# Kernel optimization log

Hardware: AMD Instinct MI355X
Metric: run time of the kernel (lower is better)

## Reference

```python
import jax, jax.numpy as jnp
import numpy as np

N = 1_000_000
HID = 128

def setup_inputs() -> dict:
    key = jax.random.key(0)
    ks = jax.random.split(key, 4)
    F = jnp.eye(2, dtype=jnp.float32)[None] + 0.1 * jax.random.normal(ks[0], (N, 2, 2), dtype=jnp.float32)
    W1 = jax.random.normal(ks[1], (7, HID), dtype=jnp.float32) * (1.0 / np.sqrt(7))
    b1 = jnp.zeros((HID,), dtype=jnp.float32)
    W2 = jax.random.normal(ks[2], (HID, HID), dtype=jnp.float32) * (1.0 / np.sqrt(HID))
    b2 = jnp.zeros((HID,), dtype=jnp.float32)
    W3 = jax.random.normal(ks[3], (HID, 4), dtype=jnp.float32) * (1.0 / np.sqrt(HID))
    b3 = jnp.zeros((4,), dtype=jnp.float32)
    return {"F": F, "W1": W1, "b1": b1, "W2": W2, "b2": b2, "W3": W3, "b3": b3}

def reference(F, W1, b1, W2, b2, W3, b3):
    F = F.reshape(-1, 2, 2)                      # [N,2,2]
    U, sigma, Vh = jnp.linalg.svd(F)             # batched 2x2 SVD
    R = jnp.matmul(U, Vh)                        # rotation part, [N,2,2]
    FtF = jnp.einsum('nij,nik->njk', F, F)       # F^T F, [N,2,2]
    I = jnp.eye(2, dtype=F.dtype)
    I1 = sigma - 1.0                             # [N,2]
    I2 = (FtF - I).reshape(-1, 4)                # [N,4]
    det = F[:, 0, 0] * F[:, 1, 1] - F[:, 0, 1] * F[:, 1, 0]
    I3 = det[:, None] - 1.0                      # [N,1]
    inv = jnp.concatenate([I1, I2, I3], axis=1)  # [N,7]
    h = jax.nn.relu(inv @ W1 + b1)
    h = jax.nn.relu(h @ W2 + b2)
    x = (h @ W3 + b3).reshape(-1, 2, 2)
    x = (x + jnp.swapaxes(x, 1, 2)) * 0.5        # symmetrize
    delta_Fp = jnp.matmul(R, x)
    return delta_Fp + F
```

## Files before the change

### kernel.cpp

```cpp
#include <hip/hip_runtime.h>

typedef _Float16 f16x8 __attribute__((ext_vector_type(8)));
typedef _Float16 f16x2 __attribute__((ext_vector_type(2)));
typedef __fp16   fp16x2r __attribute__((ext_vector_type(2)));
typedef float    f32x4 __attribute__((ext_vector_type(4)));

#define MFMA(a, b, c) __builtin_amdgcn_mfma_f32_16x16x32_f16((a), (b), (c), 0, 0, 0)

__device__ inline f16x8 zero8() {
    f16x8 z;
#pragma unroll
    for (int i = 0; i < 8; ++i) z[i] = (_Float16)0.0f;
    return z;
}

__global__ __launch_bounds__(256, 1)
void DeformationCorrector_78967268704761_kernel(
        const float* __restrict__ F,
        const float* __restrict__ W1, const float* __restrict__ b1,
        const float* __restrict__ W2, const float* __restrict__ b2,
        const float* __restrict__ W3, const float* __restrict__ b3,
        float* __restrict__ out, int N)
{
    __shared__ __align__(16) _Float16 W2f[8][4][64][8];
    __shared__ __align__(16) _Float16 W1f[8][16][8];
    __shared__ __align__(16) _Float16 W3c[4][16][8];
    __shared__ __align__(16) _Float16 invL[256][8];
    __shared__ __align__(16) _Float16 scratch[4][64][40];

    const int tid  = threadIdx.x;
    const int lane = tid & 63;
    const int w    = tid >> 6;
    const int l15  = tid & 15;
    const int quad = (tid >> 4) & 3;

    for (int m = tid; m < 128 * 128; m += 256) {
        int k = m >> 7, n = m & 127;
        W2f[n >> 4][k >> 5][((k >> 3) & 3) * 16 + (n & 15)][k & 7] = (_Float16)W2[m];
    }
    for (int f = tid; f < 1024; f += 256) {
        int nt = f >> 7, n15 = (f >> 3) & 15, j = f & 7;
        W1f[nt][n15][j] = (_Float16)((j < 7) ? W1[j * 128 + nt * 16 + n15]
                                             : b1[nt * 16 + n15]);
    }
    for (int f = tid; f < 512; f += 256) {
        int s = f >> 7, idx = (f >> 3) & 15, j = f & 7;
        int q = idx >> 2, n3 = idx & 3;
        int ch = s * 32 + (j & 1) * 16 + q * 4 + (j >> 1);
        W3c[s][idx][j] = (_Float16)W3[ch * 4 + n3];
    }
    float b2r[8];
#pragma unroll
    for (int nt = 0; nt < 8; ++nt) b2r[nt] = b2[nt * 16 + l15];
    const float b3v = (l15 < 4) ? b3[l15] : 0.f;
    __syncthreads();

    const int ntiles = (N + 255) >> 8;
    const int stride = (int)gridDim.x;

    float a, b, c, d;
    {
        const int p0 = blockIdx.x * 256 + tid;
        if (blockIdx.x < ntiles && p0 < N) {
            const float4 f4 = *(const float4*)(F + 4ll * p0);
            a = f4.x; b = f4.y; c = f4.z; d = f4.w;
        } else { a = 1.f; b = 0.f; c = 0.f; d = 1.f; }
    }

    for (int tile = blockIdx.x; tile < ntiles; tile += stride) {
        float na = 1.f, nb = 0.f, nc = 0.f, nd = 1.f;
        {
            const int pn = (tile + stride) * 256 + tid;
            if (tile + stride < ntiles && pn < N) {
                const float4 f4 = *(const float4*)(F + 4ll * pn);
                na = f4.x; nb = f4.y; nc = f4.z; nd = f4.w;
            }
        }
        const int p = tile * 256 + tid;

        const float x1 = a + d, y1 = c - b, x2 = a - d, y2 = c + b;
        const float h1v = sqrtf(x1 * x1 + y1 * y1);
        const float h2v = sqrtf(x2 * x2 + y2 * y2);
        const float s1 = 0.5f * (h1v + h2v), s2 = 0.5f * (h1v - h2v);
        const float ir = 1.0f / h1v;
        const float Rc = x1 * ir, Rs = y1 * ir;
        f16x8 iv;
        iv[0] = (_Float16)(s1 - 1.f);
        iv[1] = (_Float16)(s2 - 1.f);
        iv[2] = (_Float16)(a * a + c * c - 1.f);
        const float i3 = a * b + c * d;
        iv[3] = (_Float16)i3;
        iv[4] = (_Float16)i3;
        iv[5] = (_Float16)(b * b + d * d - 1.f);
        iv[6] = (_Float16)(a * d - b * c - 1.f);
        iv[7] = (_Float16)1.0f;
        *(f16x8*)(&invL[tid][0]) = iv;

        f16x8 binv[4];
#pragma unroll
        for (int mt = 0; mt < 4; ++mt)
            binv[mt] = (quad == 0) ? *(const f16x8*)(&invL[w * 64 + mt * 16 + l15][0])
                                   : zero8();

        f32x4 acc2[8][4];
#pragma unroll
        for (int nt2 = 0; nt2 < 8; ++nt2)
#pragma unroll
            for (int mt2 = 0; mt2 < 4; ++mt2) acc2[nt2][mt2] = (f32x4){0.f, 0.f, 0.f, 0.f};

        for (int ks = 0; ks < 4; ++ks) {
#pragma unroll
            for (int h = 0; h < 2; ++h) {
                const f16x8 bw1 = (lane < 16) ? *(const f16x8*)(&W1f[2 * ks + h][l15][0])
                                              : zero8();
#pragma unroll
                for (int mt = 0; mt < 4; ++mt) {
                    f32x4 cz = {0.f, 0.f, 0.f, 0.f};
                    const f32x4 cc = MFMA(binv[mt], bw1, cz);
#pragma unroll
                    for (int r = 0; r < 4; ++r)
                        scratch[w][mt * 16 + quad * 4 + r][h * 16 + l15] =
                            (_Float16)fmaxf(cc[r], 0.f);
                }
            }
            f16x8 af[4];
#pragma unroll
            for (int mt2 = 0; mt2 < 4; ++mt2)
                af[mt2] = *(const f16x8*)(&scratch[w][mt2 * 16 + l15][quad * 8]);
#pragma unroll
            for (int nt2 = 0; nt2 < 8; ++nt2) {
                const f16x8 bf = *(const f16x8*)(&W2f[nt2][ks][lane][0]);
#pragma unroll
                for (int mt2 = 0; mt2 < 4; ++mt2)
                    acc2[nt2][mt2] = MFMA(af[mt2], bf, acc2[nt2][mt2]);
            }
        }

        f32x4 acc3[4];
#pragma unroll
        for (int mt2 = 0; mt2 < 4; ++mt2) acc3[mt2] = (f32x4){0.f, 0.f, 0.f, 0.f};

#pragma unroll
        for (int s = 0; s < 4; ++s) {
            const float bb0 = b2r[2 * s], bb1 = b2r[2 * s + 1];
#pragma unroll
            for (int mt2 = 0; mt2 < 4; ++mt2)
#pragma unroll
                for (int r = 0; r < 4; ++r) {
                    const fp16x2r pwr = __builtin_amdgcn_cvt_pkrtz(
                        fmaxf(acc2[2 * s + 0][mt2][r] + bb0, 0.f),
                        fmaxf(acc2[2 * s + 1][mt2][r] + bb1, 0.f));
                    *(f16x2*)(&scratch[w][mt2 * 16 + quad * 4 + r][2 * l15]) =
                        __builtin_bit_cast(f16x2, pwr);
                }
            const f16x8 bw3 = (l15 < 4) ? *(const f16x8*)(&W3c[s][quad * 4 + l15][0])
                                        : zero8();
#pragma unroll
            for (int mt2 = 0; mt2 < 4; ++mt2) {
                const f16x8 ah = *(const f16x8*)(&scratch[w][mt2 * 16 + l15][quad * 8]);
                acc3[mt2] = MFMA(ah, bw3, acc3[mt2]);
            }
        }

        float* xf = (float*)(&scratch[w][0][0]);
#pragma unroll
        for (int mt2 = 0; mt2 < 4; ++mt2)
#pragma unroll
            for (int r = 0; r < 4; ++r)
                if (l15 < 4)
                    xf[(mt2 * 16 + quad * 4 + r) * 4 + l15] = acc3[mt2][r] + b3v;

        const float4 xv = *(const float4*)(&xf[lane * 4]);
        const float xm  = 0.5f * (xv.y + xv.z);
        const float d00 = Rc * xv.x - Rs * xm;
        const float d01 = Rc * xm   - Rs * xv.w;
        const float d10 = Rs * xv.x + Rc * xm;
        const float d11 = Rs * xm   + Rc * xv.w;
        if (p < N) {
            float4 o;
            o.x = a + d00; o.y = b + d01; o.z = c + d10; o.w = d + d11;
            *(float4*)(out + 4ll * p) = o;
        }

        a = na; b = nb; c = nc; d = nd;
    }
}

extern "C" void kernel_launch(void* const* d_in, const int* in_sizes, int n_in,
                              void* d_out, int out_size, void* d_ws, size_t ws_size,
                              hipStream_t stream) {
    const float* F  = (const float*)d_in[0];
    const float* W1 = (const float*)d_in[1];
    const float* b1 = (const float*)d_in[2];
    const float* W2 = (const float*)d_in[3];
    const float* b2 = (const float*)d_in[4];
    const float* W3 = (const float*)d_in[5];
    const float* b3 = (const float*)d_in[6];
    float* out = (float*)d_out;
    const int N = in_sizes[0] / 4;
    const int ntiles = (N + 255) / 256;
    const int grid = ntiles < 512 ? ntiles : 512;
    DeformationCorrector_78967268704761_kernel<<<grid, 256, 0, stream>>>(
        F, W1, b1, W2, b2, W3, b3, out, N);
}
```

Before: 136.7 us.

## Compute MLP transposed so activations stay in registers between MFMA layers

Swaps the MFMA operand roles so weights become the A operand and per-particle activations the B operand. Each layer's accumulator output then lands directly in the register layout the next MFMA needs, so the LDS scratch round-trips between layers go away. Biases b2 and b3 are now loaded into the accumulator initial values instead of added afterwards. W2 and W3 are permuted in LDS to match the new layout. This removes LDS writes, reads and barriers-like traffic, but the 16 live B2 fragments raise register pressure.

```diff
diff --git a/kernel.cpp b/kernel.cpp
--- a/kernel.cpp
+++ b/kernel.cpp
@@ -1,7 +1,6 @@
 #include <hip/hip_runtime.h>
 
 typedef _Float16 f16x8 __attribute__((ext_vector_type(8)));
-typedef _Float16 f16x2 __attribute__((ext_vector_type(2)));
 typedef __fp16   fp16x2r __attribute__((ext_vector_type(2)));
 typedef float    f32x4 __attribute__((ext_vector_type(4)));
 
@@ -12,6 +11,26 @@
 #pragma unroll
     for (int i = 0; i < 8; ++i) z[i] = (_Float16)0.0f;
     return z;
+}
+
+__device__ inline f16x8 relu_pack8_rtn(f32x4 lo, f32x4 hi) {
+    f16x8 v;
+#pragma unroll
+    for (int i = 0; i < 4; ++i) {
+        v[i]     = (_Float16)fmaxf(lo[i], 0.f);
+        v[i + 4] = (_Float16)fmaxf(hi[i], 0.f);
+    }
+    return v;
+}
+
+__device__ inline f16x8 relu_pack8_rtz(f32x4 lo, f32x4 hi) {
+    const fp16x2r p0 = __builtin_amdgcn_cvt_pkrtz(fmaxf(lo[0], 0.f), fmaxf(lo[1], 0.f));
+    const fp16x2r p1 = __builtin_amdgcn_cvt_pkrtz(fmaxf(lo[2], 0.f), fmaxf(lo[3], 0.f));
+    const fp16x2r p2 = __builtin_amdgcn_cvt_pkrtz(fmaxf(hi[0], 0.f), fmaxf(hi[1], 0.f));
+    const fp16x2r p3 = __builtin_amdgcn_cvt_pkrtz(fmaxf(hi[2], 0.f), fmaxf(hi[3], 0.f));
+    uint4 u = { __builtin_bit_cast(unsigned int, p0), __builtin_bit_cast(unsigned int, p1),
+                __builtin_bit_cast(unsigned int, p2), __builtin_bit_cast(unsigned int, p3) };
+    return __builtin_bit_cast(f16x8, u);
 }
 
 __global__ __launch_bounds__(256, 1)
@@ -22,11 +41,11 @@
         const float* __restrict__ W3, const float* __restrict__ b3,
         float* __restrict__ out, int N)
 {
-    __shared__ __align__(16) _Float16 W2f[8][4][64][8];
-    __shared__ __align__(16) _Float16 W1f[8][16][8];
-    __shared__ __align__(16) _Float16 W3c[4][16][8];
-    __shared__ __align__(16) _Float16 invL[256][8];
-    __shared__ __align__(16) _Float16 scratch[4][64][40];
+    __shared__ __align__(16) _Float16 W2A[8][4][64][8];
+    __shared__ __align__(16) _Float16 W1A[8][16][8];
+    __shared__ __align__(16) _Float16 W3A[4][16][8];
+    __shared__ __align__(16) float    b2L[128];
+    __shared__ __align__(16) _Float16 invL[4][64][8];
 
     const int tid  = threadIdx.x;
     const int lane = tid & 63;
@@ -35,24 +54,27 @@
     const int quad = (tid >> 4) & 3;
 
     for (int m = tid; m < 128 * 128; m += 256) {
-        int k = m >> 7, n = m & 127;
-        W2f[n >> 4][k >> 5][((k >> 3) & 3) * 16 + (n & 15)][k & 7] = (_Float16)W2[m];
+        const int k = m >> 7, n = m & 127;
+        const int s = k >> 5, j = ((k >> 4) & 1) * 4 + (k & 3), q = (k >> 2) & 3;
+        W2A[n >> 4][s][q * 16 + (n & 15)][j] = (_Float16)W2[m];
     }
     for (int f = tid; f < 1024; f += 256) {
-        int nt = f >> 7, n15 = (f >> 3) & 15, j = f & 7;
-        W1f[nt][n15][j] = (_Float16)((j < 7) ? W1[j * 128 + nt * 16 + n15]
-                                             : b1[nt * 16 + n15]);
+        const int mt = f >> 7, n15 = (f >> 3) & 15, j = f & 7;
+        W1A[mt][n15][j] = (_Float16)((j < 7) ? W1[j * 128 + mt * 16 + n15]
+                                             : b1[mt * 16 + n15]);
     }
     for (int f = tid; f < 512; f += 256) {
-        int s = f >> 7, idx = (f >> 3) & 15, j = f & 7;
-        int q = idx >> 2, n3 = idx & 3;
-        int ch = s * 32 + (j & 1) * 16 + q * 4 + (j >> 1);
-        W3c[s][idx][j] = (_Float16)W3[ch * 4 + n3];
-    }
-    float b2r[8];
-#pragma unroll
-    for (int nt = 0; nt < 8; ++nt) b2r[nt] = b2[nt * 16 + l15];
-    const float b3v = (l15 < 4) ? b3[l15] : 0.f;
+        const int s3 = f >> 7, idx = (f >> 3) & 15, j = f & 7;
+        const int q = idx >> 2, c3 = idx & 3;
+        const int ch2 = (2 * s3 + (j >> 2)) * 16 + q * 4 + (j & 3);
+        W3A[s3][idx][j] = (_Float16)W3[ch2 * 4 + c3];
+    }
+    if (tid < 128) b2L[tid] = b2[tid];
+    f32x4 b3i;
+    {
+        const float4 t = *(const float4*)b3;
+        b3i = (quad == 0) ? (f32x4){t.x, t.y, t.z, t.w} : (f32x4){0.f, 0.f, 0.f, 0.f};
+    }
     __syncthreads();
 
     const int ntiles = (N + 255) >> 8;
@@ -94,88 +116,69 @@
         iv[5] = (_Float16)(b * b + d * d - 1.f);
         iv[6] = (_Float16)(a * d - b * c - 1.f);
         iv[7] = (_Float16)1.0f;
-        *(f16x8*)(&invL[tid][0]) = iv;
-
-        f16x8 binv[4];
-#pragma unroll
-        for (int mt = 0; mt < 4; ++mt)
-            binv[mt] = (quad == 0) ? *(const f16x8*)(&invL[w * 64 + mt * 16 + l15][0])
-                                   : zero8();
-
-        f32x4 acc2[8][4];
-#pragma unroll
-        for (int nt2 = 0; nt2 < 8; ++nt2)
-#pragma unroll
-            for (int mt2 = 0; mt2 < 4; ++mt2) acc2[nt2][mt2] = (f32x4){0.f, 0.f, 0.f, 0.f};
-
-        for (int ks = 0; ks < 4; ++ks) {
-#pragma unroll
-            for (int h = 0; h < 2; ++h) {
-                const f16x8 bw1 = (lane < 16) ? *(const f16x8*)(&W1f[2 * ks + h][l15][0])
-                                              : zero8();
-#pragma unroll
-                for (int mt = 0; mt < 4; ++mt) {
-                    f32x4 cz = {0.f, 0.f, 0.f, 0.f};
-                    const f32x4 cc = MFMA(binv[mt], bw1, cz);
-#pragma unroll
-                    for (int r = 0; r < 4; ++r)
-                        scratch[w][mt * 16 + quad * 4 + r][h * 16 + l15] =
-                            (_Float16)fmaxf(cc[r], 0.f);
+        *(f16x8*)(&invL[w][lane][0]) = iv;
+
+        f16x8 B1[4];
+#pragma unroll
+        for (int nt = 0; nt < 4; ++nt)
+            B1[nt] = (quad == 0) ? *(const f16x8*)(&invL[w][nt * 16 + l15][0]) : zero8();
+
+        f16x8 B2[4][4];
+#pragma unroll
+        for (int s = 0; s < 4; ++s) {
+            const f16x8 aLo = (quad == 0) ? *(const f16x8*)(&W1A[2 * s][l15][0])     : zero8();
+            const f16x8 aHi = (quad == 0) ? *(const f16x8*)(&W1A[2 * s + 1][l15][0]) : zero8();
+#pragma unroll
+            for (int nt = 0; nt < 4; ++nt) {
+                const f32x4 cz  = {0.f, 0.f, 0.f, 0.f};
+                const f32x4 dLo = MFMA(aLo, B1[nt], cz);
+                const f32x4 dHi = MFMA(aHi, B1[nt], cz);
+                B2[s][nt] = relu_pack8_rtn(dLo, dHi);
+            }
+        }
+
+        f32x4 acc3[4];
+#pragma unroll
+        for (int nt = 0; nt < 4; ++nt) acc3[nt] = b3i;
+
+#pragma unroll
+        for (int s3 = 0; s3 < 4; ++s3) {
+            f32x4 accE[4], accO[4];
+            {
+                const f32x4 bvE = *(const f32x4*)(&b2L[(2 * s3) * 16 + quad * 4]);
+                const f32x4 bvO = *(const f32x4*)(&b2L[(2 * s3 + 1) * 16 + quad * 4]);
+#pragma unroll
+                for (int nt = 0; nt < 4; ++nt) { accE[nt] = bvE; accO[nt] = bvO; }
+            }
+#pragma unroll
+            for (int s = 0; s < 4; ++s) {
+                const f16x8 aE = *(const f16x8*)(&W2A[2 * s3][s][lane][0]);
+                const f16x8 aO = *(const f16x8*)(&W2A[2 * s3 + 1][s][lane][0]);
+#pragma unroll
+                for (int nt = 0; nt < 4; ++nt) {
+                    accE[nt] = MFMA(aE, B2[s][nt], accE[nt]);
+                    accO[nt] = MFMA(aO, B2[s][nt], accO[nt]);
                 }
             }
-            f16x8 af[4];
-#pragma unroll
-            for (int mt2 = 0; mt2 < 4; ++mt2)
-                af[mt2] = *(const f16x8*)(&scratch[w][mt2 * 16 + l15][quad * 8]);
-#pragma unroll
-            for (int nt2 = 0; nt2 < 8; ++nt2) {
-                const f16x8 bf = *(const f16x8*)(&W2f[nt2][ks][lane][0]);
-#pragma unroll
-                for (int mt2 = 0; mt2 < 4; ++mt2)
-                    acc2[nt2][mt2] = MFMA(af[mt2], bf, acc2[nt2][mt2]);
-            }
-        }
-
-        f32x4 acc3[4];
-#pragma unroll
-        for (int mt2 = 0; mt2 < 4; ++mt2) acc3[mt2] = (f32x4){0.f, 0.f, 0.f, 0.f};
-
-#pragma unroll
-        for (int s = 0; s < 4; ++s) {
-            const float bb0 = b2r[2 * s], bb1 = b2r[2 * s + 1];
-#pragma unroll
-            for (int mt2 = 0; mt2 < 4; ++mt2)
-#pragma unroll
-                for (int r = 0; r < 4; ++r) {
-                    const fp16x2r pwr = __builtin_amdgcn_cvt_pkrtz(
-                        fmaxf(acc2[2 * s + 0][mt2][r] + bb0, 0.f),
-                        fmaxf(acc2[2 * s + 1][mt2][r] + bb1, 0.f));
-                    *(f16x2*)(&scratch[w][mt2 * 16 + quad * 4 + r][2 * l15]) =
-                        __builtin_bit_cast(f16x2, pwr);
-                }
-            const f16x8 bw3 = (l15 < 4) ? *(const f16x8*)(&W3c[s][quad * 4 + l15][0])
-                                        : zero8();
-#pragma unroll
-            for (int mt2 = 0; mt2 < 4; ++mt2) {
-                const f16x8 ah = *(const f16x8*)(&scratch[w][mt2 * 16 + l15][quad * 8]);
-                acc3[mt2] = MFMA(ah, bw3, acc3[mt2]);
-            }
-        }
-
-        float* xf = (float*)(&scratch[w][0][0]);
-#pragma unroll
-        for (int mt2 = 0; mt2 < 4; ++mt2)
-#pragma unroll
-            for (int r = 0; r < 4; ++r)
-                if (l15 < 4)
-                    xf[(mt2 * 16 + quad * 4 + r) * 4 + l15] = acc3[mt2][r] + b3v;
-
-        const float4 xv = *(const float4*)(&xf[lane * 4]);
-        const float xm  = 0.5f * (xv.y + xv.z);
-        const float d00 = Rc * xv.x - Rs * xm;
-        const float d01 = Rc * xm   - Rs * xv.w;
-        const float d10 = Rs * xv.x + Rc * xm;
-        const float d11 = Rs * xm   + Rc * xv.w;
+            const f16x8 a3 = (l15 < 4) ? *(const f16x8*)(&W3A[s3][quad * 4 + l15][0]) : zero8();
+#pragma unroll
+            for (int nt = 0; nt < 4; ++nt) {
+                const f16x8 b3f = relu_pack8_rtz(accE[nt], accO[nt]);
+                acc3[nt] = MFMA(a3, b3f, acc3[nt]);
+            }
+        }
+
+        if (quad == 0) {
+#pragma unroll
+            for (int nt = 0; nt < 4; ++nt)
+                *(f16x8*)(&invL[w][nt * 16 + l15][0]) = __builtin_bit_cast(f16x8, acc3[nt]);
+        }
+        const f32x4 xv = __builtin_bit_cast(f32x4, *(const f16x8*)(&invL[w][lane][0]));
+        const float xm  = 0.5f * (xv[1] + xv[2]);
+        const float d00 = Rc * xv[0] - Rs * xm;
+        const float d01 = Rc * xm    - Rs * xv[3];
+        const float d10 = Rs * xv[0] + Rc * xm;
+        const float d11 = Rs * xm    + Rc * xv[3];
         if (p < N) {
             float4 o;
             o.x = a + d00; o.y = b + d01; o.z = c + d10; o.w = d + d11;
```

New measurement: 141.8 us. +3.8%, slower.
